# Kernel tuning notes

Measured on AMD Instinct MI355X. Metric: run time of the kernel, lower is better.

## Reference

```python
import jax, jax.numpy as jnp
import numpy as np

N, E, F_IN, DIM, HEADS = 16384, 262144, 128, 64, 4
HID = DIM * HEADS  # 256
NEG = 0.2


def _lin(k, fan_in, fan_out):
    kw, kb = jax.random.split(k)
    s = 1.0 / np.sqrt(fan_in)
    return (jax.random.uniform(kw, (fan_in, fan_out), jnp.float32, -s, s),
            jax.random.uniform(kb, (fan_out,), jnp.float32, -s, s))


def setup_inputs() -> dict:
    key = jax.random.key(0)
    ks = jax.random.split(key, 20)
    x = jax.random.normal(ks[0], (N, F_IN), jnp.float32)
    edge_index = jax.random.randint(ks[1], (2, E), 0, N, jnp.int32)
    Win, b_in = _lin(ks[2], F_IN, DIM)
    Wskip, bskip = _lin(ks[3], DIM, HID)
    # conv1: in=DIM, out per head=DIM, heads=HEADS, concat -> HID
    Wl1, _ = _lin(ks[4], DIM, HID)
    Wr1, _ = _lin(ks[5], DIM, HID)
    att1 = jax.random.normal(ks[6], (HEADS, DIM), jnp.float32) * 0.1
    b1 = jnp.zeros((HID,), jnp.float32)
    # conv2: in=HID, out=HID, heads=1, concat=False
    Wl2, _ = _lin(ks[7], HID, HID)
    Wr2, _ = _lin(ks[8], HID, HID)
    att2 = jax.random.normal(ks[9], (1, HID), jnp.float32) * 0.1
    b2 = jnp.zeros((HID,), jnp.float32)
    # conv3: in=HID, out=HID, heads=1, concat=False
    Wl3, _ = _lin(ks[10], HID, HID)
    Wr3, _ = _lin(ks[11], HID, HID)
    att3 = jax.random.normal(ks[12], (1, HID), jnp.float32) * 0.1
    b3 = jnp.zeros((HID,), jnp.float32)
    Wm1, bm1 = _lin(ks[13], HID, DIM)
    Wm2, bm2 = _lin(ks[14], DIM, DIM)
    Wm3, bm3 = _lin(ks[15], DIM, 1)
    return dict(x=x, edge_index=edge_index, Win=Win, b_in=b_in,
                Wskip=Wskip, bskip=bskip,
                Wl1=Wl1, Wr1=Wr1, att1=att1, b1=b1,
                Wl2=Wl2, Wr2=Wr2, att2=att2, b2=b2,
                Wl3=Wl3, Wr3=Wr3, att3=att3, b3=b3,
                Wm1=Wm1, bm1=bm1, Wm2=Wm2, bm2=bm2, Wm3=Wm3, bm3=bm3)


def gatv2(x, src, dst, Wl, Wr, att, b, concat):
    # PyG GATv2Conv: x_l = lin_l(x)[src], x_r = lin_r(x)[dst]
    n = x.shape[0]
    H, D = att.shape
    xl = (x @ Wl).reshape(n, H, D)
    xr = (x @ Wr).reshape(n, H, D)
    e = jax.nn.leaky_relu(xl[src] + xr[dst], NEG)          # [E, H, D]
    logits = jnp.einsum('ehd,hd->eh', e, att)              # [E, H]
    m = jax.ops.segment_max(logits, dst, num_segments=n)   # per-dst softmax
    alpha = jnp.exp(logits - m[dst])
    denom = jax.ops.segment_sum(alpha, dst, num_segments=n)
    alpha = alpha / denom[dst]
    out = jax.ops.segment_sum(alpha[:, :, None] * xl[src], dst, num_segments=n)
    out = out.reshape(n, H * D) if concat else out.mean(axis=1)
    return out + b


def reference(x, edge_index, Win, b_in, Wskip, bskip,
              Wl1, Wr1, att1, b1, Wl2, Wr2, att2, b2,
              Wl3, Wr3, att3, b3, Wm1, bm1, Wm2, bm2, Wm3, bm3):
    n = x.shape[0]
    # add self loops (GATv2Conv default add_self_loops=True)
    loop = jnp.arange(n, dtype=edge_index.dtype)
    src = jnp.concatenate([edge_index[0], loop])
    dst = jnp.concatenate([edge_index[1], loop])

    h = jax.nn.relu(x @ Win + b_in)                         # [N, DIM]
    out1 = jax.nn.relu(gatv2(h, src, dst, Wl1, Wr1, att1, b1, True))
    out1 = out1 + (h @ Wskip + bskip)                       # [N, HID]
    out2 = jax.nn.relu(gatv2(out1, src, dst, Wl2, Wr2, att2, b2, False))
    out2 = out2 + out1
    out3 = jax.nn.relu(gatv2(out2, src, dst, Wl3, Wr3, att3, b3, False))
    out3 = out3 + out2
    out = jax.nn.relu(out3 @ Wm1 + bm1)
    out = jax.nn.relu(out @ Wm2 + bm2)
    out = out @ Wm3 + bm3                                   # [N, 1]
    return out.reshape(-1)
```

## Files before the change

kernel.cpp:

```cpp
#include <hip/hip_runtime.h>
#include <cstdint>
#include <cstddef>

#define N_NODES 16384
#define E_EDGES 262144
#define FIN     128
#define DIM     64
#define HID     256
#define NEG     0.2f

typedef _Float16 h8 __attribute__((ext_vector_type(8)));
typedef _Float16 h4 __attribute__((ext_vector_type(4)));
typedef float    f32x4 __attribute__((ext_vector_type(4)));

__global__ __launch_bounds__(256) void hist_kernel(const int* __restrict__ dst,
                                                   int* __restrict__ cnt) {
    int i = blockIdx.x * 256 + threadIdx.x;
    if (i < E_EDGES) atomicAdd(&cnt[dst[i]], 1);
}

__global__ __launch_bounds__(256) void csr_scan_kernel(const int* __restrict__ cnt,
                                                       int* __restrict__ offs,
                                                       int* __restrict__ cursor) {
    __shared__ int bs[256];
    __shared__ int psum[257];
    int tid = threadIdx.x;
    int base = tid * 64;
    int s = 0;
    for (int i = 0; i < 64; ++i) s += cnt[base + i];
    bs[tid] = s;
    __syncthreads();
    if (tid == 0) {
        int r = 0;
        for (int i = 0; i < 256; ++i) { psum[i] = r; r += bs[i]; }
        psum[256] = r;
    }
    __syncthreads();
    int run = psum[tid];
    for (int i = 0; i < 64; ++i) {
        int c = cnt[base + i];
        offs[base + i] = run;
        cursor[base + i] = run;
        run += c;
    }
    if (tid == 255) offs[N_NODES] = run;
}

__global__ __launch_bounds__(256) void scatter_kernel(const int* __restrict__ src,
                                                      const int* __restrict__ dst,
                                                      int* __restrict__ cursor,
                                                      int* __restrict__ esrc) {
    int i = blockIdx.x * 256 + threadIdx.x;
    if (i < E_EDGES) {
        int p = atomicAdd(&cursor[dst[i]], 1);
        esrc[p] = src[i];
    }
}

__global__ __launch_bounds__(256) void pack_w_kernel(const float* __restrict__ W,
                                                     _Float16* __restrict__ Wp,
                                                     int Ksrc, int Nsrc, int NT, int colOff) {
    int i = blockIdx.x * 256 + threadIdx.x;
    if (i < Ksrc * Nsrc) {
        int k = i / Nsrc, n = i % Nsrc;
        Wp[((size_t)(k >> 3) * NT + colOff + n) * 8 + (k & 7)] = (_Float16)W[i];
    }
}

template<bool RELU, bool HASB, bool O16>
__global__ __launch_bounds__(256) void gemm_kernel(const float* __restrict__ A,
                                                   const float* __restrict__ W,
                                                   const float* __restrict__ bias,
                                                   void* __restrict__ Cv,
                                                   int K, int M) {
    __shared__ float As[16][68];
    __shared__ float Bs[16][64];
    int tid = threadIdx.x;
    int rowBase = blockIdx.x * 64;
    int colBase = blockIdx.y * 64;
    int tx = tid & 15, ty = tid >> 4;

    int ar = tid >> 2;
    int ak = (tid & 3) * 4;
    int bk = tid >> 4;
    int bm = (tid & 15) * 4;

    float acc[4][4] = {};
    for (int kb = 0; kb < K; kb += 16) {
        float4 a4 = *(const float4*)(A + (size_t)(rowBase + ar) * K + kb + ak);
        As[ak + 0][ar] = a4.x; As[ak + 1][ar] = a4.y;
        As[ak + 2][ar] = a4.z; As[ak + 3][ar] = a4.w;
        *(float4*)&Bs[bk][bm] = *(const float4*)(W + (size_t)(kb + bk) * M + colBase + bm);
        __syncthreads();
#pragma unroll
        for (int k = 0; k < 16; ++k) {
            float4 a4r = *(const float4*)&As[k][ty * 4];
            float4 b4r = *(const float4*)&Bs[k][tx * 4];
            float a[4] = {a4r.x, a4r.y, a4r.z, a4r.w};
            float b[4] = {b4r.x, b4r.y, b4r.z, b4r.w};
#pragma unroll
            for (int i = 0; i < 4; ++i)
#pragma unroll
                for (int j = 0; j < 4; ++j) acc[i][j] += a[i] * b[j];
        }
        __syncthreads();
    }
#pragma unroll
    for (int i = 0; i < 4; ++i) {
#pragma unroll
        for (int j = 0; j < 4; ++j) {
            int col = colBase + tx * 4 + j;
            float v = acc[i][j];
            if (HASB) v += bias[col];
            if (RELU) v = fmaxf(v, 0.f);
            size_t idx = (size_t)(rowBase + ty * 4 + i) * M + col;
            if constexpr (O16) ((_Float16*)Cv)[idx] = (_Float16)v;
            else               ((float*)Cv)[idx] = v;
        }
    }
}

template<int K>
__global__ __launch_bounds__(256) void mfma_gemm_kernel(const _Float16* __restrict__ A,
                                                        const _Float16* __restrict__ Wp,
                                                        int NT,
                                                        _Float16* __restrict__ o16a,
                                                        _Float16* __restrict__ o16b,
                                                        float* __restrict__ o32,
                                                        const float* __restrict__ bias) {
    int tid = threadIdx.x;
    int lane = tid & 63, wid = tid >> 6;
    int wm = wid >> 1, wn = wid & 1;
    int rowBase = blockIdx.x * 128 + wm * 64;
    int colBase = blockIdx.y * 128 + wn * 64;
    int l15 = lane & 15, l4 = lane >> 4;

    f32x4 acc[4][4] = {};

#pragma unroll
    for (int ks = 0; ks < K / 32; ++ks) {
        h8 af[4], bf[4];
#pragma unroll
        for (int mi = 0; mi < 4; ++mi)
            af[mi] = *(const h8*)(A + (size_t)(rowBase + mi * 16 + l15) * K + ks * 32 + l4 * 8);
#pragma unroll
        for (int ni = 0; ni < 4; ++ni)
            bf[ni] = *(const h8*)(Wp + ((size_t)(ks * 4 + l4) * NT + colBase + ni * 16 + l15) * 8);
#pragma unroll
        for (int mi = 0; mi < 4; ++mi)
#pragma unroll
            for (int ni = 0; ni < 4; ++ni)
                acc[mi][ni] = __builtin_amdgcn_mfma_f32_16x16x32_f16(af[mi], bf[ni], acc[mi][ni], 0, 0, 0);
    }

    int seg = colBase >> 8;
    int cbase = colBase & 255;
    if (o32 != nullptr && seg == 2) {
#pragma unroll
        for (int mi = 0; mi < 4; ++mi)
#pragma unroll
            for (int ni = 0; ni < 4; ++ni) {
                int c = cbase + ni * 16 + l15;
                float bv = bias[c];
#pragma unroll
                for (int q = 0; q < 4; ++q) {
                    int r = rowBase + mi * 16 + l4 * 4 + q;
                    o32[(size_t)r * 256 + c] = acc[mi][ni][q] + bv;
                }
            }
    } else {
        _Float16* o = (seg == 0) ? o16a : o16b;
#pragma unroll
        for (int mi = 0; mi < 4; ++mi)
#pragma unroll
            for (int ni = 0; ni < 4; ++ni) {
                int c = cbase + ni * 16 + l15;
#pragma unroll
                for (int q = 0; q < 4; ++q) {
                    int r = rowBase + mi * 16 + l4 * 4 + q;
                    o[(size_t)r * 256 + c] = (_Float16)acc[mi][ni][q];
                }
            }
    }
}

template<int H, bool W16>
__global__ __launch_bounds__(256) void gat_agg_kernel(const _Float16* __restrict__ xl,
                                                      const _Float16* __restrict__ xr,
                                                      const float* __restrict__ att,
                                                      const float* __restrict__ bias,
                                                      const float* __restrict__ resid,
                                                      const int* __restrict__ offs,
                                                      const int* __restrict__ esrc,
                                                      float* __restrict__ out,
                                                      _Float16* __restrict__ out16) {
    int wid = threadIdx.x >> 6;
    int lane = threadIdx.x & 63;
    int node = blockIdx.x * 4 + wid;

    auto ld4 = [&](const _Float16* p, int n) -> float4 {
        h4 v = *(const h4*)(p + ((size_t)n << 8) + (lane << 2));
        return make_float4((float)v[0], (float)v[1], (float)v[2], (float)v[3]);
    };

    float4 xrv = ld4(xr, node);
    float4 av = ((const float4*)att)[lane];

    float m = -1e30f, s = 0.f;
    float4 acc = make_float4(0.f, 0.f, 0.f, 0.f);

    auto logit = [&](const float4& xlv) -> float {
        float ex = xlv.x + xrv.x; ex = ex > 0.f ? ex : NEG * ex;
        float ey = xlv.y + xrv.y; ey = ey > 0.f ? ey : NEG * ey;
        float ez = xlv.z + xrv.z; ez = ez > 0.f ? ez : NEG * ez;
        float ew = xlv.w + xrv.w; ew = ew > 0.f ? ew : NEG * ew;
        float lp = ex * av.x + ey * av.y + ez * av.z + ew * av.w;
        lp += __shfl_xor(lp, 1);
        lp += __shfl_xor(lp, 2);
        lp += __shfl_xor(lp, 4);
        lp += __shfl_xor(lp, 8);
        if constexpr (H == 1) {
            lp += __shfl_xor(lp, 16);
            lp += __shfl_xor(lp, 32);
        }
        return lp;
    };

    auto single = [&](int src) {
        float4 xlv = ld4(xl, src);
        float lp = logit(xlv);
        float mn = fmaxf(m, lp);
        float c = __expf(m - mn);
        float p = __expf(lp - mn);
        s = s * c + p;
        acc.x = acc.x * c + p * xlv.x;
        acc.y = acc.y * c + p * xlv.y;
        acc.z = acc.z * c + p * xlv.z;
        acc.w = acc.w * c + p * xlv.w;
        m = mn;
    };

    single(node);
    int e0 = offs[node], e1 = offs[node + 1];
    int e = e0;
    for (; e + 4 <= e1; e += 4) {
        int s0 = esrc[e], s1 = esrc[e + 1], s2 = esrc[e + 2], s3 = esrc[e + 3];
        float4 x0 = ld4(xl, s0);
        float4 x1 = ld4(xl, s1);
        float4 x2 = ld4(xl, s2);
        float4 x3 = ld4(xl, s3);
        float lp0 = logit(x0);
        float lp1 = logit(x1);
        float lp2 = logit(x2);
        float lp3 = logit(x3);
        float mn = fmaxf(fmaxf(fmaxf(lp0, lp1), fmaxf(lp2, lp3)), m);
        float c  = __expf(m - mn);
        float p0 = __expf(lp0 - mn);
        float p1 = __expf(lp1 - mn);
        float p2 = __expf(lp2 - mn);
        float p3 = __expf(lp3 - mn);
        s = s * c + ((p0 + p1) + (p2 + p3));
        acc.x = acc.x * c + ((p0 * x0.x + p1 * x1.x) + (p2 * x2.x + p3 * x3.x));
        acc.y = acc.y * c + ((p0 * x0.y + p1 * x1.y) + (p2 * x2.y + p3 * x3.y));
        acc.z = acc.z * c + ((p0 * x0.z + p1 * x1.z) + (p2 * x2.z + p3 * x3.z));
        acc.w = acc.w * c + ((p0 * x0.w + p1 * x1.w) + (p2 * x2.w + p3 * x3.w));
        m = mn;
    }
    for (; e < e1; ++e) single(esrc[e]);

    float inv = 1.f / s;
    float4 bv = ((const float4*)bias)[lane];
    float4 rv = ((const float4*)resid)[((size_t)node << 6) + lane];
    float4 o;
    o.x = fmaxf(acc.x * inv + bv.x, 0.f) + rv.x;
    o.y = fmaxf(acc.y * inv + bv.y, 0.f) + rv.y;
    o.z = fmaxf(acc.z * inv + bv.z, 0.f) + rv.z;
    o.w = fmaxf(acc.w * inv + bv.w, 0.f) + rv.w;
    ((float4*)out)[((size_t)node << 6) + lane] = o;
    if constexpr (W16) {
        h4 ov;
        ov[0] = (_Float16)o.x; ov[1] = (_Float16)o.y;
        ov[2] = (_Float16)o.z; ov[3] = (_Float16)o.w;
        *(h4*)(out16 + ((size_t)node << 8) + (lane << 2)) = ov;
    }
}

__global__ __launch_bounds__(256) void mlp_final_kernel(const float* __restrict__ A,
                                                        const float* __restrict__ w,
                                                        const float* __restrict__ b,
                                                        float* __restrict__ out) {
    int wid = threadIdx.x >> 6;
    int lane = threadIdx.x & 63;
    int node = blockIdx.x * 4 + wid;
    float v = A[((size_t)node << 6) + lane] * w[lane];
    v += __shfl_xor(v, 1);
    v += __shfl_xor(v, 2);
    v += __shfl_xor(v, 4);
    v += __shfl_xor(v, 8);
    v += __shfl_xor(v, 16);
    v += __shfl_xor(v, 32);
    if (lane == 0) out[node] = v + b[0];
}

extern "C" void kernel_launch(void* const* d_in, const int* in_sizes, int n_in,
                              void* d_out, int out_size, void* d_ws, size_t ws_size,
                              hipStream_t stream) {
    const float* x     = (const float*)d_in[0];
    const int*   ei    = (const int*)d_in[1];
    const float* Win   = (const float*)d_in[2];
    const float* b_in  = (const float*)d_in[3];
    const float* Wskip = (const float*)d_in[4];
    const float* bskip = (const float*)d_in[5];
    const float* Wl1   = (const float*)d_in[6];
    const float* Wr1   = (const float*)d_in[7];
    const float* att1  = (const float*)d_in[8];
    const float* b1    = (const float*)d_in[9];
    const float* Wl2   = (const float*)d_in[10];
    const float* Wr2   = (const float*)d_in[11];
    const float* att2  = (const float*)d_in[12];
    const float* b2    = (const float*)d_in[13];
    const float* Wl3   = (const float*)d_in[14];
    const float* Wr3   = (const float*)d_in[15];
    const float* att3  = (const float*)d_in[16];
    const float* b3    = (const float*)d_in[17];
    const float* Wm1   = (const float*)d_in[18];
    const float* bm1   = (const float*)d_in[19];
    const float* Wm2   = (const float*)d_in[20];
    const float* bm2   = (const float*)d_in[21];
    const float* Wm3   = (const float*)d_in[22];
    const float* bm3   = (const float*)d_in[23];

    char* p = (char*)d_ws;
    auto alloc = [&](size_t bytes) { char* r = p; p += (bytes + 255) & ~(size_t)255; return r; };
    const size_t NN = N_NODES;
    float*    tA   = (float*)alloc(NN * 64 * 4);
    float*    tB   = (float*)alloc(NN * 64 * 4);
    float*    skip = (float*)alloc(NN * 256 * 4);
    float*    out1 = (float*)alloc(NN * 256 * 4);
    _Float16* o116 = (_Float16*)alloc(NN * 256 * 2);
    _Float16* o216 = (_Float16*)alloc(NN * 256 * 2);
    float*    out3 = (float*)o116;
    _Float16* h16  = (_Float16*)alloc(NN * 64 * 2);
    _Float16* xl16 = (_Float16*)alloc(NN * 256 * 2);
    _Float16* xr16 = (_Float16*)alloc(NN * 256 * 2);
    _Float16* Wp1  = (_Float16*)alloc((size_t)64 * 768 * 2);
    _Float16* Wp2  = (_Float16*)alloc((size_t)256 * 512 * 2);
    _Float16* Wp3  = (_Float16*)alloc((size_t)256 * 512 * 2);
    int* cnt    = (int*)alloc(N_NODES * 4);
    int* offs   = (int*)alloc((N_NODES + 1) * 4);
    int* cursor = (int*)alloc(N_NODES * 4);
    int* esrc   = (int*)alloc(E_EDGES * 4);

    const int* src = ei;
    const int* dst = ei + E_EDGES;

    hipMemsetAsync(cnt, 0, N_NODES * sizeof(int), stream);
    hist_kernel<<<E_EDGES / 256, 256, 0, stream>>>(dst, cnt);
    csr_scan_kernel<<<1, 256, 0, stream>>>(cnt, offs, cursor);
    scatter_kernel<<<E_EDGES / 256, 256, 0, stream>>>(src, dst, cursor, esrc);

    int pg = (64 * 256 + 255) / 256;
    pack_w_kernel<<<pg, 256, 0, stream>>>(Wl1, Wp1, 64, 256, 768, 0);
    pack_w_kernel<<<pg, 256, 0, stream>>>(Wr1, Wp1, 64, 256, 768, 256);
    pack_w_kernel<<<pg, 256, 0, stream>>>(Wskip, Wp1, 64, 256, 768, 512);
    int pg2 = (256 * 256 + 255) / 256;
    pack_w_kernel<<<pg2, 256, 0, stream>>>(Wl2, Wp2, 256, 256, 512, 0);
    pack_w_kernel<<<pg2, 256, 0, stream>>>(Wr2, Wp2, 256, 256, 512, 256);
    pack_w_kernel<<<pg2, 256, 0, stream>>>(Wl3, Wp3, 256, 256, 512, 0);
    pack_w_kernel<<<pg2, 256, 0, stream>>>(Wr3, Wp3, 256, 256, 512, 256);

    gemm_kernel<true, true, true><<<dim3(256, 1), 256, 0, stream>>>(x, Win, b_in, h16, FIN, DIM);

    mfma_gemm_kernel<64><<<dim3(128, 6), 256, 0, stream>>>(h16, Wp1, 768, xl16, xr16, skip, bskip);
    gat_agg_kernel<4, true><<<N_NODES / 4, 256, 0, stream>>>(xl16, xr16, att1, b1, skip, offs, esrc, out1, o116);

    mfma_gemm_kernel<256><<<dim3(128, 4), 256, 0, stream>>>(o116, Wp2, 512, xl16, xr16, nullptr, nullptr);
    gat_agg_kernel<1, true><<<N_NODES / 4, 256, 0, stream>>>(xl16, xr16, att2, b2, out1, offs, esrc, skip , o216);

    mfma_gemm_kernel<256><<<dim3(128, 4), 256, 0, stream>>>(o216, Wp3, 512, xl16, xr16, nullptr, nullptr);
    gat_agg_kernel<1, false><<<N_NODES / 4, 256, 0, stream>>>(xl16, xr16, att3, b3, skip , offs, esrc, out3, nullptr);

    gemm_kernel<true, true, false><<<dim3(256, 1), 256, 0, stream>>>(out3, Wm1, bm1, tA, HID, DIM);
    gemm_kernel<true, true, false><<<dim3(256, 1), 256, 0, stream>>>(tA, Wm2, bm2, tB, DIM, DIM);
    mlp_final_kernel<<<N_NODES / 4, 256, 0, stream>>>(tB, Wm3, bm3, (float*)d_out);
}
```

Measured before the change: 238.5 us.

## Move small GEMMs to MFMA, batch weight packing, fuse final MLP layers

The fp32 tiled GEMMs for the input projection and the first MLP layer are replaced with fp16 MFMA kernels; this needs a new cast pass over x and fp16 packing of Win and Wm1. The seven weight-pack launches become a single batched launch, the memset becomes a small zero kernel, and the layer-3 aggregation writes only fp16 output. The last two MLP layers are fused into one kernel that keeps Wm2 in shared memory, dropping an intermediate buffer and several launches. Running these layers in fp16 reduces precision.

```diff
diff --git a/kernel.cpp b/kernel.cpp
--- a/kernel.cpp
+++ b/kernel.cpp
@@ -12,6 +12,10 @@
 typedef _Float16 h8 __attribute__((ext_vector_type(8)));
 typedef _Float16 h4 __attribute__((ext_vector_type(4)));
 typedef float    f32x4 __attribute__((ext_vector_type(4)));
+
+__global__ __launch_bounds__(256) void zero_cnt_kernel(int4* __restrict__ cnt) {
+    cnt[blockIdx.x * 256 + threadIdx.x] = make_int4(0, 0, 0, 0);
+}
 
 __global__ __launch_bounds__(256) void hist_kernel(const int* __restrict__ dst,
                                                    int* __restrict__ cnt) {
@@ -57,67 +61,68 @@
     }
 }
 
-__global__ __launch_bounds__(256) void pack_w_kernel(const float* __restrict__ W,
-                                                     _Float16* __restrict__ Wp,
-                                                     int Ksrc, int Nsrc, int NT, int colOff) {
+struct PackJob { const float* W; _Float16* dst; int Ksrc, Nsrc, NT, colOff; };
+struct PackJobs { PackJob j[9]; };
+
+__global__ __launch_bounds__(256) void pack_all_kernel(PackJobs jobs) {
+    PackJob jb = jobs.j[blockIdx.y];
     int i = blockIdx.x * 256 + threadIdx.x;
-    if (i < Ksrc * Nsrc) {
-        int k = i / Nsrc, n = i % Nsrc;
-        Wp[((size_t)(k >> 3) * NT + colOff + n) * 8 + (k & 7)] = (_Float16)W[i];
-    }
-}
-
-template<bool RELU, bool HASB, bool O16>
-__global__ __launch_bounds__(256) void gemm_kernel(const float* __restrict__ A,
-                                                   const float* __restrict__ W,
-                                                   const float* __restrict__ bias,
-                                                   void* __restrict__ Cv,
-                                                   int K, int M) {
-    __shared__ float As[16][68];
-    __shared__ float Bs[16][64];
+    if (i < jb.Ksrc * jb.Nsrc) {
+        int k = i / jb.Nsrc, n = i % jb.Nsrc;
+        jb.dst[((size_t)(k >> 3) * jb.NT + jb.colOff + n) * 8 + (k & 7)] = (_Float16)jb.W[i];
+    }
+}
+
+__global__ __launch_bounds__(256) void cast16_kernel(const float* __restrict__ x,
+                                                     _Float16* __restrict__ x16) {
+    int i = blockIdx.x * 256 + threadIdx.x;
+    float4 v = ((const float4*)x)[i];
+    h4 o; o[0] = (_Float16)v.x; o[1] = (_Float16)v.y;
+    o[2] = (_Float16)v.z; o[3] = (_Float16)v.w;
+    ((h4*)x16)[i] = o;
+}
+
+template<int K, bool RELU, bool O16>
+__global__ __launch_bounds__(256) void mfma_nt64_kernel(const _Float16* __restrict__ A,
+                                                        const _Float16* __restrict__ Wp,
+                                                        const float* __restrict__ bias,
+                                                        void* __restrict__ outv) {
     int tid = threadIdx.x;
-    int rowBase = blockIdx.x * 64;
-    int colBase = blockIdx.y * 64;
-    int tx = tid & 15, ty = tid >> 4;
-
-    int ar = tid >> 2;
-    int ak = (tid & 3) * 4;
-    int bk = tid >> 4;
-    int bm = (tid & 15) * 4;
-
-    float acc[4][4] = {};
-    for (int kb = 0; kb < K; kb += 16) {
-        float4 a4 = *(const float4*)(A + (size_t)(rowBase + ar) * K + kb + ak);
-        As[ak + 0][ar] = a4.x; As[ak + 1][ar] = a4.y;
-        As[ak + 2][ar] = a4.z; As[ak + 3][ar] = a4.w;
-        *(float4*)&Bs[bk][bm] = *(const float4*)(W + (size_t)(kb + bk) * M + colBase + bm);
-        __syncthreads();
-#pragma unroll
-        for (int k = 0; k < 16; ++k) {
-            float4 a4r = *(const float4*)&As[k][ty * 4];
-            float4 b4r = *(const float4*)&Bs[k][tx * 4];
-            float a[4] = {a4r.x, a4r.y, a4r.z, a4r.w};
-            float b[4] = {b4r.x, b4r.y, b4r.z, b4r.w};
-#pragma unroll
-            for (int i = 0; i < 4; ++i)
-#pragma unroll
-                for (int j = 0; j < 4; ++j) acc[i][j] += a[i] * b[j];
+    int lane = tid & 63, wid = tid >> 6;
+    int rowBase = blockIdx.x * 256 + wid * 64;
+    int l15 = lane & 15, l4 = lane >> 4;
+
+    f32x4 acc[4][4] = {};
+#pragma unroll
+    for (int ks = 0; ks < K / 32; ++ks) {
+        h8 af[4], bf[4];
+#pragma unroll
+        for (int mi = 0; mi < 4; ++mi)
+            af[mi] = *(const h8*)(A + (size_t)(rowBase + mi * 16 + l15) * K + ks * 32 + l4 * 8);
+#pragma unroll
+        for (int ni = 0; ni < 4; ++ni)
+            bf[ni] = *(const h8*)(Wp + ((size_t)(ks * 4 + l4) * 64 + ni * 16 + l15) * 8);
+#pragma unroll
+        for (int mi = 0; mi < 4; ++mi)
+#pragma unroll
+            for (int ni = 0; ni < 4; ++ni)
+                acc[mi][ni] = __builtin_amdgcn_mfma_f32_16x16x32_f16(af[mi], bf[ni], acc[mi][ni], 0, 0, 0);
+    }
+#pragma unroll
+    for (int mi = 0; mi < 4; ++mi)
+#pragma unroll
+        for (int ni = 0; ni < 4; ++ni) {
+            int c = ni * 16 + l15;
+            float bv = bias[c];
+#pragma unroll
+            for (int q = 0; q < 4; ++q) {
+                int r = rowBase + mi * 16 + l4 * 4 + q;
+                float v = acc[mi][ni][q] + bv;
+                if (RELU) v = fmaxf(v, 0.f);
+                if constexpr (O16) ((_Float16*)outv)[(size_t)r * 64 + c] = (_Float16)v;
+                else               ((float*)outv)[(size_t)r * 64 + c] = v;
+            }
         }
-        __syncthreads();
-    }
-#pragma unroll
-    for (int i = 0; i < 4; ++i) {
-#pragma unroll
-        for (int j = 0; j < 4; ++j) {
-            int col = colBase + tx * 4 + j;
-            float v = acc[i][j];
-            if (HASB) v += bias[col];
-            if (RELU) v = fmaxf(v, 0.f);
-            size_t idx = (size_t)(rowBase + ty * 4 + i) * M + col;
-            if constexpr (O16) ((_Float16*)Cv)[idx] = (_Float16)v;
-            else               ((float*)Cv)[idx] = v;
-        }
-    }
 }
 
 template<int K>
@@ -136,7 +141,6 @@
     int l15 = lane & 15, l4 = lane >> 4;
 
     f32x4 acc[4][4] = {};
-
 #pragma unroll
     for (int ks = 0; ks < K / 32; ++ks) {
         h8 af[4], bf[4];
@@ -184,7 +188,7 @@
     }
 }
 
-template<int H, bool W16>
+template<int H, int OMODE>
 __global__ __launch_bounds__(256) void gat_agg_kernel(const _Float16* __restrict__ xl,
                                                       const _Float16* __restrict__ xr,
                                                       const float* __restrict__ att,
@@ -276,8 +280,9 @@
     o.y = fmaxf(acc.y * inv + bv.y, 0.f) + rv.y;
     o.z = fmaxf(acc.z * inv + bv.z, 0.f) + rv.z;
     o.w = fmaxf(acc.w * inv + bv.w, 0.f) + rv.w;
-    ((float4*)out)[((size_t)node << 6) + lane] = o;
-    if constexpr (W16) {
+    if constexpr (OMODE != 2)
+        ((float4*)out)[((size_t)node << 6) + lane] = o;
+    if constexpr (OMODE != 0) {
         h4 ov;
         ov[0] = (_Float16)o.x; ov[1] = (_Float16)o.y;
         ov[2] = (_Float16)o.z; ov[3] = (_Float16)o.w;
@@ -285,21 +290,37 @@
     }
 }
 
-__global__ __launch_bounds__(256) void mlp_final_kernel(const float* __restrict__ A,
-                                                        const float* __restrict__ w,
-                                                        const float* __restrict__ b,
-                                                        float* __restrict__ out) {
-    int wid = threadIdx.x >> 6;
-    int lane = threadIdx.x & 63;
-    int node = blockIdx.x * 4 + wid;
-    float v = A[((size_t)node << 6) + lane] * w[lane];
-    v += __shfl_xor(v, 1);
-    v += __shfl_xor(v, 2);
-    v += __shfl_xor(v, 4);
-    v += __shfl_xor(v, 8);
-    v += __shfl_xor(v, 16);
-    v += __shfl_xor(v, 32);
-    if (lane == 0) out[node] = v + b[0];
+__global__ __launch_bounds__(256) void mlp23_kernel(const float* __restrict__ tA,
+                                                    const float* __restrict__ Wm2,
+                                                    const float* __restrict__ bm2,
+                                                    const float* __restrict__ Wm3,
+                                                    const float* __restrict__ bm3,
+                                                    float* __restrict__ out) {
+    __shared__ float W2s[64][65];
+    __shared__ float w3s[64];
+    int tid = threadIdx.x;
+    for (int i = tid; i < 4096; i += 256) W2s[i >> 6][i & 63] = Wm2[i];
+    if (tid < 64) w3s[tid] = Wm3[tid];
+    __syncthreads();
+    int wid = tid >> 6, lane = tid & 63;
+    float b2 = bm2[lane];
+    float b3 = bm3[0];
+#pragma unroll 1
+    for (int i = 0; i < 8; ++i) {
+        int node = blockIdx.x * 32 + wid * 8 + i;
+        float a = tA[((size_t)node << 6) + lane];
+        float accv = 0.f;
+#pragma unroll
+        for (int k = 0; k < 64; ++k) accv += __shfl(a, k) * W2s[k][lane];
+        float o = fmaxf(accv + b2, 0.f) * w3s[lane];
+        o += __shfl_xor(o, 1);
+        o += __shfl_xor(o, 2);
+        o += __shfl_xor(o, 4);
+        o += __shfl_xor(o, 8);
+        o += __shfl_xor(o, 16);
+        o += __shfl_xor(o, 32);
+        if (lane == 0) out[node] = o + b3;
+    }
 }
 
 extern "C" void kernel_launch(void* const* d_in, const int* in_sizes, int n_in,
@@ -334,18 +355,20 @@
     auto alloc = [&](size_t bytes) { char* r = p; p += (bytes + 255) & ~(size_t)255; return r; };
     const size_t NN = N_NODES;
     float*    tA   = (float*)alloc(NN * 64 * 4);
-    float*    tB   = (float*)alloc(NN * 64 * 4);
     float*    skip = (float*)alloc(NN * 256 * 4);
     float*    out1 = (float*)alloc(NN * 256 * 4);
     _Float16* o116 = (_Float16*)alloc(NN * 256 * 2);
     _Float16* o216 = (_Float16*)alloc(NN * 256 * 2);
-    float*    out3 = (float*)o116;
+    _Float16* o316 = o116;
     _Float16* h16  = (_Float16*)alloc(NN * 64 * 2);
+    _Float16* x16  = (_Float16*)alloc(NN * FIN * 2);
     _Float16* xl16 = (_Float16*)alloc(NN * 256 * 2);
     _Float16* xr16 = (_Float16*)alloc(NN * 256 * 2);
     _Float16* Wp1  = (_Float16*)alloc((size_t)64 * 768 * 2);
     _Float16* Wp2  = (_Float16*)alloc((size_t)256 * 512 * 2);
     _Float16* Wp3  = (_Float16*)alloc((size_t)256 * 512 * 2);
+    _Float16* Winp = (_Float16*)alloc((size_t)128 * 64 * 2);
+    _Float16* Wm1p = (_Float16*)alloc((size_t)256 * 64 * 2);
     int* cnt    = (int*)alloc(N_NODES * 4);
     int* offs   = (int*)alloc((N_NODES + 1) * 4);
     int* cursor = (int*)alloc(N_NODES * 4);
@@ -354,33 +377,36 @@
     const int* src = ei;
     const int* dst = ei + E_EDGES;
 
-    hipMemsetAsync(cnt, 0, N_NODES * sizeof(int), stream);
+    zero_cnt_kernel<<<N_NODES / 1024, 256, 0, stream>>>((int4*)cnt);
     hist_kernel<<<E_EDGES / 256, 256, 0, stream>>>(dst, cnt);
     csr_scan_kernel<<<1, 256, 0, stream>>>(cnt, offs, cursor);
     scatter_kernel<<<E_EDGES / 256, 256, 0, stream>>>(src, dst, cursor, esrc);
 
-    int pg = (64 * 256 + 255) / 256;
-    pack_w_kernel<<<pg, 256, 0, stream>>>(Wl1, Wp1, 64, 256, 768, 0);
-    pack_w_kernel<<<pg, 256, 0, stream>>>(Wr1, Wp1, 64, 256, 768, 256);
-    pack_w_kernel<<<pg, 256, 0, stream>>>(Wskip, Wp1, 64, 256, 768, 512);
-    int pg2 = (256 * 256 + 255) / 256;
-    pack_w_kernel<<<pg2, 256, 0, stream>>>(Wl2, Wp2, 256, 256, 512, 0);
-    pack_w_kernel<<<pg2, 256, 0, stream>>>(Wr2, Wp2, 256, 256, 512, 256);
-    pack_w_kernel<<<pg2, 256, 0, stream>>>(Wl3, Wp3, 256, 256, 512, 0);
-    pack_w_kernel<<<pg2, 256, 0, stream>>>(Wr3, Wp3, 256, 256, 512, 256);
-
-    gemm_kernel<true, true, true><<<dim3(256, 1), 256, 0, stream>>>(x, Win, b_in, h16, FIN, DIM);
+    PackJobs jobs = {{
+        { Wl1,   Wp1,  64,  256, 768, 0   },
+        { Wr1,   Wp1,  64,  256, 768, 256 },
+        { Wskip, Wp1,  64,  256, 768, 512 },
+        { Wl2,   Wp2,  256, 256, 512, 0   },
+        { Wr2,   Wp2,  256, 256, 512, 256 },
+        { Wl3,   Wp3,  256, 256, 512, 0   },
+        { Wr3,   Wp3,  256, 256, 512, 256 },
+        { Win,   Winp, 128, 64,  64,  0   },
+        { Wm1,   Wm1p, 256, 64,  64,  0   },
+    }};
+    pack_all_kernel<<<dim3(256, 9), 256, 0, stream>>>(jobs);
+
+    cast16_kernel<<<(N_NODES * FIN / 4) / 256, 256, 0, stream>>>(x, x16);
+    mfma_nt64_kernel<128, true, true><<<N_NODES / 256, 256, 0, stream>>>(x16, Winp, b_in, h16);
 
     mfma_gemm_kernel<64><<<dim3(128, 6), 256, 0, stream>>>(h16, Wp1, 768, xl16, xr16, skip, bskip);
-    gat_agg_kernel<4, true><<<N_NODES / 4, 256, 0, stream>>>(xl16, xr16, att1, b1, skip, offs, esrc, out1, o116);
+    gat_agg_kernel<4, 1><<<N_NODES / 4, 256, 0, stream>>>(xl16, xr16, att1, b1, skip, offs, esrc, out1, o116);
 
     mfma_gemm_kernel<256><<<dim3(128, 4), 256, 0, stream>>>(o116, Wp2, 512, xl16, xr16, nullptr, nullptr);
-    gat_agg_kernel<1, true><<<N_NODES / 4, 256, 0, stream>>>(xl16, xr16, att2, b2, out1, offs, esrc, skip , o216);
+    gat_agg_kernel<1, 1><<<N_NODES / 4, 256, 0, stream>>>(xl16, xr16, att2, b2, out1, offs, esrc, skip , o216);
 
     mfma_gemm_kernel<256><<<dim3(128, 4), 256, 0, stream>>>(o216, Wp3, 512, xl16, xr16, nullptr, nullptr);
-    gat_agg_kernel<1, false><<<N_NODES / 4, 256, 0, stream>>>(xl16, xr16, att3, b3, skip , offs, esrc, out3, nullptr);
-
-    gemm_kernel<true, true, false><<<dim3(256, 1), 256, 0, stream>>>(out3, Wm1, bm1, tA, HID, DIM);
-    gemm_kernel<true, true, false><<<dim3(256, 1), 256, 0, stream>>>(tA, Wm2, bm2, tB, DIM, DIM);
-    mlp_final_kernel<<<N_NODES / 4, 256, 0, stream>>>(tB, Wm3, bm3, (float*)d_out);
-}
+    gat_agg_kernel<1, 2><<<N_NODES / 4, 256, 0, stream>>>(xl16, xr16, att3, b3, skip , offs, esrc, nullptr, o316);
+
+    mfma_nt64_kernel<256, true, false><<<N_NODES / 256, 256, 0, stream>>>(o316, Wm1p, bm1, tA);
+    mlp23_kernel<<<N_NODES / 32, 256, 0, stream>>>(tA, Wm2, bm2, Wm3, bm3, (float*)d_out);
+}
```

Result: faster. 228.0 us (-4.4%).
